# Performance work log

Measured on AMD Instinct MI355X. Metric: run time of the kernel, lower is better.

## Reference

```python
import jax, jax.numpy as jnp
import numpy as np

B, N, C, HEADS = 4, 8192, 512, 8


def setup_inputs() -> dict:
    key = jax.random.key(0)
    k1, k2, k3, k4, k5 = jax.random.split(key, 5)
    s = 1.0 / np.sqrt(C)
    return {
        "x": jax.random.normal(k1, (B, N, C), dtype=jnp.float32),
        "w_qkv": jax.random.normal(k2, (3 * C, C), dtype=jnp.float32) * s,
        "b_qkv": jax.random.normal(k3, (3 * C,), dtype=jnp.float32) * 0.01,
        "w_fc": jax.random.normal(k4, (C, C), dtype=jnp.float32) * s,
        "b_fc": jax.random.normal(k5, (C,), dtype=jnp.float32) * 0.01,
        "heads": HEADS,
    }


def reference(x, w_qkv, b_qkv, w_fc, b_fc, heads):
    b, n, c = x.shape
    d = c // heads
    scale = d ** (-0.5)
    # torch Linear: y = x @ W.T + b
    qkv = (x @ w_qkv.T + b_qkv).reshape(b, n, 3, heads, d)
    q, k, v = qkv[:, :, 0], qkv[:, :, 1], qkv[:, :, 2]  # [b,n,h,d]
    # NOTE: source does NOT move heads to dim 1, so attention is over the
    # heads axis: dots is [b, n, h, h].
    dots = jnp.einsum("bnhd,bngd->bnhg", q, k) * scale
    dots = jnp.clip(dots, -50.0, 50.0)
    attn = jax.nn.softmax(dots, axis=-1)
    out = jnp.einsum("bnhg,bngd->bnhd", attn, v)  # [b,n,h,d]
    # transpose(1,2).reshape(B,N,C) exactly as in torch (scrambles n/h)
    out = out.transpose(0, 2, 1, 3).reshape(b, n, c)
    return out @ w_fc.T + b_fc
```

## Files before the change

### kernel.cpp

```cpp
#include <hip/hip_runtime.h>
#include <hip/hip_bf16.h>
#include <stdint.h>


typedef __bf16 bf16x8 __attribute__((ext_vector_type(8)));
typedef float f32x4 __attribute__((ext_vector_type(4)));

__device__ __forceinline__ unsigned short f2bf(float f) {
  unsigned u = __float_as_uint(f);
  u += 0x7fffu + ((u >> 16) & 1u);
  return (unsigned short)(u >> 16);
}
__device__ __forceinline__ unsigned pk2(float a, float b) {
  return (unsigned)f2bf(a) | ((unsigned)f2bf(b) << 16);
}
__device__ __forceinline__ void unpk2(unsigned u, float& a, float& b) {
  a = __uint_as_float(u << 16);
  b = __uint_as_float(u & 0xffff0000u);
}

__device__ __forceinline__ void gload_lds16(const void* g, void* l) {
  __builtin_amdgcn_global_load_lds((const __attribute__((address_space(1))) void*)g,
                                   (__attribute__((address_space(3))) void*)l,
                                   16, 0, 0);
}

__global__ __launch_bounds__(256) void cvt_f32_to_bf16(const float* __restrict__ in,
                                                       __hip_bfloat16* __restrict__ out,
                                                       int n8) {
  int i = blockIdx.x * 256 + threadIdx.x;
  if (i >= n8) return;
  const float4* p = (const float4*)in;
  float4 a = p[i * 2];
  float4 b = p[i * 2 + 1];
  uint4 o;
  o.x = pk2(a.x, a.y);
  o.y = pk2(a.z, a.w);
  o.z = pk2(b.x, b.y);
  o.w = pk2(b.z, b.w);
  ((uint4*)out)[i] = o;
}

template <bool OUT_BF16>
__global__ __launch_bounds__(256) void gemm_bt(const __hip_bfloat16* __restrict__ A,
                                               const __hip_bfloat16* __restrict__ Bm,
                                               const float* __restrict__ bias,
                                               void* __restrict__ C,
                                               int M, int N, int K, int NT) {
  __shared__ __hip_bfloat16 sA[128 * 64];
  __shared__ __hip_bfloat16 sB[128 * 64];

  const int tid = threadIdx.x;
  const int wv = tid >> 6;
  const int ln = tid & 63;
  const int bid = blockIdx.x;
  const int mt = bid / NT, nt = bid % NT;
  const int bm0 = mt * 128, bn0 = nt * 128;
  const int lrow = ln & 15;
  const int kg = ln >> 4;
  const int wm = wv >> 1, wn = wv & 1;

  f32x4 acc[4][4] = {};

  int srow[4], scol[4], sbase[4];
  for (int i = 0; i < 4; ++i) {
    int ofs = (i * 4 + wv) * 1024 + ln * 16;
    srow[i] = ofs >> 7;
    scol[i] = (ofs & 127) >> 1;
    sbase[i] = (i * 4 + wv) * 512;
  }

  for (int k0 = 0; k0 < K; k0 += 64) {
    for (int i = 0; i < 4; ++i) {
      gload_lds16(A + (size_t)(bm0 + srow[i]) * K + k0 + scol[i], sA + sbase[i]);
      gload_lds16(Bm + (size_t)(bn0 + srow[i]) * K + k0 + scol[i], sB + sbase[i]);
    }
    __syncthreads();
#pragma unroll
    for (int ks = 0; ks < 2; ++ks) {
      bf16x8 af[4], bfr[4];
#pragma unroll
      for (int i = 0; i < 4; ++i) {
        af[i] = *(const bf16x8*)(sA + (wm * 64 + i * 16 + lrow) * 64 + ks * 32 + kg * 8);
        bfr[i] = *(const bf16x8*)(sB + (wn * 64 + i * 16 + lrow) * 64 + ks * 32 + kg * 8);
      }
#pragma unroll
      for (int i = 0; i < 4; ++i)
#pragma unroll
        for (int j = 0; j < 4; ++j)
          acc[i][j] = __builtin_amdgcn_mfma_f32_16x16x32_bf16(af[i], bfr[j], acc[i][j], 0, 0, 0);
    }
    __syncthreads();
  }

#pragma unroll
  for (int j = 0; j < 4; ++j) {
    int col = bn0 + wn * 64 + j * 16 + lrow;
    float bv = bias[col];
#pragma unroll
    for (int i = 0; i < 4; ++i) {
      int row0 = bm0 + wm * 64 + i * 16 + kg * 4;
#pragma unroll
      for (int r = 0; r < 4; ++r) {
        float v = acc[i][j][r] + bv;
        size_t idx = (size_t)(row0 + r) * N + col;
        if (OUT_BF16) {
          unsigned short us = f2bf(v);
          ((unsigned short*)C)[idx] = us;
        } else {
          ((float*)C)[idx] = v;
        }
      }
    }
  }
}

__global__ __launch_bounds__(256) void attn_tok(const __hip_bfloat16* __restrict__ qkv,
                                                __hip_bfloat16* __restrict__ outp,
                                                int ntok, int npb) {
  const int wv = threadIdx.x >> 6;
  const int ln = threadIdx.x & 63;
  const int t = blockIdx.x * 4 + wv;
  if (t >= ntok) return;
  const int m = ln & 7;

  const __hip_bfloat16* row = qkv + (size_t)t * 1536;
  uint4 qr = *(const uint4*)(row + ln * 8);
  uint4 kr = *(const uint4*)(row + 512 + ln * 8);
  uint4 vr = *(const uint4*)(row + 1024 + ln * 8);

  float qf[8];
  unpk2(qr.x, qf[0], qf[1]);
  unpk2(qr.y, qf[2], qf[3]);
  unpk2(qr.z, qf[4], qf[5]);
  unpk2(qr.w, qf[6], qf[7]);
  unsigned kw[4] = {kr.x, kr.y, kr.z, kr.w};
  unsigned vw[4] = {vr.x, vr.y, vr.z, vr.w};

  float dt[8];
#pragma unroll
  for (int g = 0; g < 8; ++g) {
    int src = g * 8 + m;
    float s = 0.f;
#pragma unroll
    for (int j4 = 0; j4 < 4; ++j4) {
      unsigned kk = __shfl(kw[j4], src, 64);
      float a, b;
      unpk2(kk, a, b);
      s += qf[j4 * 2] * a + qf[j4 * 2 + 1] * b;
    }
    s += __shfl_xor(s, 1, 64);
    s += __shfl_xor(s, 2, 64);
    s += __shfl_xor(s, 4, 64);
    dt[g] = s;
  }

  float mx = -1e30f;
#pragma unroll
  for (int g = 0; g < 8; ++g) {
    dt[g] = fminf(fmaxf(dt[g] * 0.125f, -50.f), 50.f);
    mx = fmaxf(mx, dt[g]);
  }
  float p[8], ssum = 0.f;
#pragma unroll
  for (int g = 0; g < 8; ++g) {
    p[g] = __expf(dt[g] - mx);
    ssum += p[g];
  }
  float inv = 1.f / ssum;

  float o[8] = {0, 0, 0, 0, 0, 0, 0, 0};
#pragma unroll
  for (int g = 0; g < 8; ++g) {
    int src = g * 8 + m;
    float ag = p[g] * inv;
#pragma unroll
    for (int j4 = 0; j4 < 4; ++j4) {
      unsigned vv = __shfl(vw[j4], src, 64);
      float a, b;
      unpk2(vv, a, b);
      o[j4 * 2] += ag * a;
      o[j4 * 2 + 1] += ag * b;
    }
  }

  const int h = ln >> 3;
  const int b = t / npb, n = t % npb;
  size_t dst = (size_t)b * npb * 512 + (size_t)(h * (npb >> 3) + (n >> 3)) * 512 +
               (size_t)((n & 7) * 64 + m * 8);
  uint4 ov;
  ov.x = pk2(o[0], o[1]);
  ov.y = pk2(o[2], o[3]);
  ov.z = pk2(o[4], o[5]);
  ov.w = pk2(o[6], o[7]);
  *(uint4*)(outp + dst) = ov;
}

extern "C" void kernel_launch(void* const* d_in, const int* in_sizes, int n_in,
                              void* d_out, int out_size, void* d_ws, size_t ws_size,
                              hipStream_t stream) {
  const float* x = (const float*)d_in[0];
  const float* w_qkv = (const float*)d_in[1];
  const float* b_qkv = (const float*)d_in[2];
  const float* w_fc = (const float*)d_in[3];
  const float* b_fc = (const float*)d_in[4];
  float* out = (float*)d_out;

  const int M = 32768;
  const int Cc = 512, N3 = 1536;

  __hip_bfloat16* xb = (__hip_bfloat16*)d_ws;
  __hip_bfloat16* wqkvb = xb + (size_t)M * Cc;
  __hip_bfloat16* wfcb = wqkvb + (size_t)N3 * Cc;
  __hip_bfloat16* qkvb = wfcb + (size_t)Cc * Cc;
  __hip_bfloat16* attb = qkvb + (size_t)M * N3;

  cvt_f32_to_bf16<<<(M * Cc / 8) / 256, 256, 0, stream>>>(x, xb, M * Cc / 8);
  cvt_f32_to_bf16<<<(N3 * Cc / 8) / 256, 256, 0, stream>>>(w_qkv, wqkvb, N3 * Cc / 8);
  cvt_f32_to_bf16<<<(Cc * Cc / 8) / 256, 256, 0, stream>>>(w_fc, wfcb, Cc * Cc / 8);

  gemm_bt<true><<<(M / 128) * (N3 / 128), 256, 0, stream>>>(xb, wqkvb, b_qkv, qkvb, M, N3, Cc,
                                                            N3 / 128);
  attn_tok<<<M / 4, 256, 0, stream>>>(qkvb, attb, M, 8192);
  gemm_bt<false><<<(M / 128) * (Cc / 128), 256, 0, stream>>>(attb, wfcb, b_fc, out, M, Cc, Cc,
                                                             Cc / 128);
}
```

Baseline: 181.9 us.

## Replace GEMM with 256x256 eight-wave double-buffered pipelined MFMA kernel

Both GEMMs now use a new kernel with 256x256 tiles, 512 threads (8 waves) and 128 KB of LDS holding two stages. Global-to-LDS loads for later k-tiles are interleaved with MFMA phases, using explicit barriers, waitcnts and priority hints. It also adds an XOR-swizzled LDS layout to avoid bank conflicts and a workgroup remap across XCDs. The aim is to hide memory latency and raise MFMA utilisation, at the cost of fewer workgroups: the fc GEMM launches only 256 blocks, and the large LDS footprint limits occupancy.

```diff
diff --git a/kernel.cpp b/kernel.cpp
--- a/kernel.cpp
+++ b/kernel.cpp
@@ -18,7 +18,6 @@
   a = __uint_as_float(u << 16);
   b = __uint_as_float(u & 0xffff0000u);
 }
-
 __device__ __forceinline__ void gload_lds16(const void* g, void* l) {
   __builtin_amdgcn_global_load_lds((const __attribute__((address_space(1))) void*)g,
                                    (__attribute__((address_space(3))) void*)l,
@@ -41,72 +40,134 @@
   ((uint4*)out)[i] = o;
 }
 
+
+#define STAGEH(SBUF, ISA, SKH, KT)                                                        \
+  do {                                                                                    \
+    const __hip_bfloat16* _sp = (ISA) ? Ag : Bg;                                          \
+    int _r0 = (ISA) ? bm0 : bn0;                                                          \
+    _Pragma("unroll") for (int _j = 0; _j < 2; ++_j) {                                    \
+      gload_lds16(_sp + (size_t)(_r0 + srow[_j]) * K + (KT) * 64 + (SKH) * 32 + skoff[_j],\
+                  lds + (SBUF) * 65536 + ((ISA) ? 0 : 32768) + (SKH) * 16384 +            \
+                      destoff[_j]);                                                       \
+    }                                                                                     \
+  } while (0)
+
+#define PHASE(BUF, KS, FH, SBUF, SISA, SKH, KT, DOW)                                      \
+  do {                                                                                    \
+    const char* _ab = lds + (BUF) * 65536 + (KS) * 16384 + wm * 8192 + (FH) * 4096 + pbase;\
+    bf16x8 _af0 = *(const bf16x8*)(_ab);                                                  \
+    bf16x8 _af1 = *(const bf16x8*)(_ab + 1024);                                           \
+    bf16x8 _af2 = *(const bf16x8*)(_ab + 2048);                                           \
+    bf16x8 _af3 = *(const bf16x8*)(_ab + 3072);                                           \
+    if (FH == 0) {                                                                        \
+      const char* _bb = lds + (BUF) * 65536 + 32768 + (KS) * 16384 + wn * 4096 + pbase;   \
+      bfr[0] = *(const bf16x8*)(_bb);                                                     \
+      bfr[1] = *(const bf16x8*)(_bb + 1024);                                              \
+      bfr[2] = *(const bf16x8*)(_bb + 2048);                                              \
+      bfr[3] = *(const bf16x8*)(_bb + 3072);                                              \
+    }                                                                                     \
+    STAGEH(SBUF, SISA, SKH, KT);                                                          \
+    __builtin_amdgcn_s_barrier();                                                         \
+    asm volatile("s_waitcnt lgkmcnt(0)" ::: "memory");                                    \
+    __builtin_amdgcn_sched_barrier(0);                                                    \
+    __builtin_amdgcn_s_setprio(1);                                                        \
+    _Pragma("unroll") for (int _c = 0; _c < 4; ++_c) {                                    \
+      acc[(FH) * 4 + 0][_c] =                                                             \
+          __builtin_amdgcn_mfma_f32_16x16x32_bf16(_af0, bfr[_c], acc[(FH) * 4 + 0][_c], 0, 0, 0); \
+      acc[(FH) * 4 + 1][_c] =                                                             \
+          __builtin_amdgcn_mfma_f32_16x16x32_bf16(_af1, bfr[_c], acc[(FH) * 4 + 1][_c], 0, 0, 0); \
+      acc[(FH) * 4 + 2][_c] =                                                             \
+          __builtin_amdgcn_mfma_f32_16x16x32_bf16(_af2, bfr[_c], acc[(FH) * 4 + 2][_c], 0, 0, 0); \
+      acc[(FH) * 4 + 3][_c] =                                                             \
+          __builtin_amdgcn_mfma_f32_16x16x32_bf16(_af3, bfr[_c], acc[(FH) * 4 + 3][_c], 0, 0, 0); \
+    }                                                                                     \
+    __builtin_amdgcn_s_setprio(0);                                                        \
+    if (DOW) {                                                                            \
+      asm volatile("s_waitcnt vmcnt(4)" ::: "memory");                                    \
+    }                                                                                     \
+    __builtin_amdgcn_s_barrier();                                                         \
+    __builtin_amdgcn_sched_barrier(0);                                                    \
+  } while (0)
+
 template <bool OUT_BF16>
-__global__ __launch_bounds__(256) void gemm_bt(const __hip_bfloat16* __restrict__ A,
-                                               const __hip_bfloat16* __restrict__ Bm,
-                                               const float* __restrict__ bias,
-                                               void* __restrict__ C,
-                                               int M, int N, int K, int NT) {
-  __shared__ __hip_bfloat16 sA[128 * 64];
-  __shared__ __hip_bfloat16 sB[128 * 64];
+__global__ __launch_bounds__(512, 2) void gemm8(const __hip_bfloat16* __restrict__ Ag,
+                                                const __hip_bfloat16* __restrict__ Bg,
+                                                const float* __restrict__ bias,
+                                                void* __restrict__ C,
+                                                int M, int N, int K, int NT) {
+  __shared__ char lds[131072];
 
   const int tid = threadIdx.x;
   const int wv = tid >> 6;
   const int ln = tid & 63;
-  const int bid = blockIdx.x;
-  const int mt = bid / NT, nt = bid % NT;
-  const int bm0 = mt * 128, bn0 = nt * 128;
   const int lrow = ln & 15;
   const int kg = ln >> 4;
-  const int wm = wv >> 1, wn = wv & 1;
-
-  f32x4 acc[4][4] = {};
-
-  int srow[4], scol[4], sbase[4];
-  for (int i = 0; i < 4; ++i) {
-    int ofs = (i * 4 + wv) * 1024 + ln * 16;
-    srow[i] = ofs >> 7;
-    scol[i] = (ofs & 127) >> 1;
-    sbase[i] = (i * 4 + wv) * 512;
-  }
-
-  for (int k0 = 0; k0 < K; k0 += 64) {
-    for (int i = 0; i < 4; ++i) {
-      gload_lds16(A + (size_t)(bm0 + srow[i]) * K + k0 + scol[i], sA + sbase[i]);
-      gload_lds16(Bm + (size_t)(bn0 + srow[i]) * K + k0 + scol[i], sB + sbase[i]);
-    }
-    __syncthreads();
-#pragma unroll
-    for (int ks = 0; ks < 2; ++ks) {
-      bf16x8 af[4], bfr[4];
-#pragma unroll
-      for (int i = 0; i < 4; ++i) {
-        af[i] = *(const bf16x8*)(sA + (wm * 64 + i * 16 + lrow) * 64 + ks * 32 + kg * 8);
-        bfr[i] = *(const bf16x8*)(sB + (wn * 64 + i * 16 + lrow) * 64 + ks * 32 + kg * 8);
-      }
-#pragma unroll
-      for (int i = 0; i < 4; ++i)
-#pragma unroll
-        for (int j = 0; j < 4; ++j)
-          acc[i][j] = __builtin_amdgcn_mfma_f32_16x16x32_bf16(af[i], bfr[j], acc[i][j], 0, 0, 0);
-    }
-    __syncthreads();
-  }
-
-#pragma unroll
-  for (int j = 0; j < 4; ++j) {
-    int col = bn0 + wn * 64 + j * 16 + lrow;
+  const int wm = wv >> 2;
+  const int wn = wv & 3;
+
+  int nwg = gridDim.x;
+  int cpx = nwg >> 3;
+  int bs = (blockIdx.x & 7) * cpx + (blockIdx.x >> 3);
+  const int bm0 = (bs / NT) * 256;
+  const int bn0 = (bs % NT) * 256;
+
+  const int pbase = (lrow >> 1) * 128 + ((((lrow & 1) << 2) | kg) ^ ((lrow >> 1) & 7)) * 16;
+
+  int srow[2], skoff[2], destoff[2];
+#pragma unroll
+  for (int j = 0; j < 2; ++j) {
+    int L = j * 8192 + wv * 1024 + ln * 16;
+    int rp = L >> 7;
+    int T = ((L >> 4) & 7) ^ (rp & 7);
+    srow[j] = rp * 2 + (T >> 2);
+    skoff[j] = (T & 3) * 8;
+    destoff[j] = j * 8192 + wv * 1024;
+  }
+
+  f32x4 acc[8][4] = {};
+  bf16x8 bfr[4];
+
+  const int NKT = K >> 6;
+  const int NI = NKT >> 1;
+
+  STAGEH(0, 1, 0, 0);
+  STAGEH(0, 0, 0, 0);
+  STAGEH(0, 1, 1, 0);
+  STAGEH(0, 0, 1, 0);
+  STAGEH(1, 1, 0, 1);
+  STAGEH(1, 0, 0, 1);
+  asm volatile("s_waitcnt vmcnt(4)" ::: "memory");
+  __builtin_amdgcn_s_barrier();
+  __builtin_amdgcn_sched_barrier(0);
+
+  for (int i = 0; i < NI; ++i) {
+    int kt1 = 2 * i + 1;
+    int kt2 = 2 * i + 2 < NKT ? 2 * i + 2 : NKT - 1;
+    int kt3 = 2 * i + 3 < NKT ? 2 * i + 3 : NKT - 1;
+    PHASE(0, 0, 0,  1, 1, 1, kt1, 0);
+    PHASE(0, 0, 1,  1, 0, 1, kt1, 0);
+    PHASE(0, 1, 0,  0, 1, 0, kt2, 0);
+    PHASE(0, 1, 1,  0, 0, 0, kt2, 1);
+    PHASE(1, 0, 0,  0, 1, 1, kt2, 0);
+    PHASE(1, 0, 1,  0, 0, 1, kt2, 0);
+    PHASE(1, 1, 0,  1, 1, 0, kt3, 0);
+    PHASE(1, 1, 1,  1, 0, 0, kt3, 1);
+  }
+  asm volatile("s_waitcnt vmcnt(0)" ::: "memory");
+
+#pragma unroll
+  for (int cj = 0; cj < 4; ++cj) {
+    int col = bn0 + wn * 64 + cj * 16 + lrow;
     float bv = bias[col];
 #pragma unroll
-    for (int i = 0; i < 4; ++i) {
-      int row0 = bm0 + wm * 64 + i * 16 + kg * 4;
+    for (int fi = 0; fi < 8; ++fi) {
+      int row0 = bm0 + wm * 128 + fi * 16 + kg * 4;
 #pragma unroll
       for (int r = 0; r < 4; ++r) {
-        float v = acc[i][j][r] + bv;
+        float v = acc[fi][cj][r] + bv;
         size_t idx = (size_t)(row0 + r) * N + col;
         if (OUT_BF16) {
-          unsigned short us = f2bf(v);
-          ((unsigned short*)C)[idx] = us;
+          ((unsigned short*)C)[idx] = f2bf(v);
         } else {
           ((float*)C)[idx] = v;
         }
@@ -219,9 +280,9 @@
   cvt_f32_to_bf16<<<(N3 * Cc / 8) / 256, 256, 0, stream>>>(w_qkv, wqkvb, N3 * Cc / 8);
   cvt_f32_to_bf16<<<(Cc * Cc / 8) / 256, 256, 0, stream>>>(w_fc, wfcb, Cc * Cc / 8);
 
-  gemm_bt<true><<<(M / 128) * (N3 / 128), 256, 0, stream>>>(xb, wqkvb, b_qkv, qkvb, M, N3, Cc,
-                                                            N3 / 128);
+  gemm8<true><<<(M / 256) * (N3 / 256), 512, 0, stream>>>(xb, wqkvb, b_qkv, qkvb, M, N3, Cc,
+                                                          N3 / 256);
   attn_tok<<<M / 4, 256, 0, stream>>>(qkvb, attb, M, 8192);
-  gemm_bt<false><<<(M / 128) * (Cc / 128), 256, 0, stream>>>(attb, wfcb, b_fc, out, M, Cc, Cc,
-                                                             Cc / 128);
-}
+  gemm8<false><<<(M / 256) * (Cc / 256), 512, 0, stream>>>(attb, wfcb, b_fc, out, M, Cc, Cc,
+                                                           Cc / 256);
+}
```

Result: faster. 168.0 us (-7.6%).

## Rewrite GEMMs with double-buffered swizzled LDS, larger tiles, and coalesced epilogue

Applied to the files above, without the earlier changes.

Replaces the single-buffered 128x128 GEMM with a 512-thread, 256x128-tile kernel. It prefetches the next 32-wide K slice into a second LDS buffer while the current one feeds MFMAs, and uses an XOR-swizzled LDS layout to avoid bank conflicts. Block IDs are remapped across 8 groups, probably for XCD-aware locality. Results are staged through LDS for vectorized, coalesced stores. This adds more LDS use and synchronization and uses a narrower K step per iteration.

```diff
diff --git a/kernel.cpp b/kernel.cpp
--- a/kernel.cpp
+++ b/kernel.cpp
@@ -18,7 +18,6 @@
   a = __uint_as_float(u << 16);
   b = __uint_as_float(u & 0xffff0000u);
 }
-
 __device__ __forceinline__ void gload_lds16(const void* g, void* l) {
   __builtin_amdgcn_global_load_lds((const __attribute__((address_space(1))) void*)g,
                                    (__attribute__((address_space(3))) void*)l,
@@ -41,76 +40,163 @@
   ((uint4*)out)[i] = o;
 }
 
+
+#define STG(S, BUF)                                                                       \
+  do {                                                                                    \
+    int _k0 = (S) * 32;                                                                   \
+    gload_lds16(Ag + (size_t)(bm0 + srowA0) * K + _k0 + skofA0,                           \
+                lds + (BUF) * 24576 + dstA0);                                             \
+    gload_lds16(Ag + (size_t)(bm0 + srowA1) * K + _k0 + skofA1,                           \
+                lds + (BUF) * 24576 + dstA1);                                             \
+    gload_lds16(Bg + (size_t)(bn0 + srowB) * K + _k0 + skofB,                             \
+                lds + (BUF) * 24576 + 16384 + dstB);                                      \
+  } while (0)
+
 template <bool OUT_BF16>
-__global__ __launch_bounds__(256) void gemm_bt(const __hip_bfloat16* __restrict__ A,
-                                               const __hip_bfloat16* __restrict__ Bm,
-                                               const float* __restrict__ bias,
-                                               void* __restrict__ C,
-                                               int M, int N, int K, int NT) {
-  __shared__ __hip_bfloat16 sA[128 * 64];
-  __shared__ __hip_bfloat16 sB[128 * 64];
+__global__ __launch_bounds__(512, 4) void gemm2p(const __hip_bfloat16* __restrict__ Ag,
+                                                 const __hip_bfloat16* __restrict__ Bg,
+                                                 const float* __restrict__ bias,
+                                                 void* __restrict__ C,
+                                                 int M, int N, int K, int NT) {
+  __shared__ __align__(16) char lds[65536];
 
   const int tid = threadIdx.x;
   const int wv = tid >> 6;
   const int ln = tid & 63;
-  const int bid = blockIdx.x;
-  const int mt = bid / NT, nt = bid % NT;
-  const int bm0 = mt * 128, bn0 = nt * 128;
   const int lrow = ln & 15;
   const int kg = ln >> 4;
-  const int wm = wv >> 1, wn = wv & 1;
+  const int wm = wv >> 1;
+  const int wn = wv & 1;
+
+  int nwg = gridDim.x;
+  int cpx = nwg >> 3;
+  int bs = (blockIdx.x & 7) * cpx + (blockIdx.x >> 3);
+  const int bm0 = (bs / NT) * 256;
+  const int bn0 = (bs % NT) * 128;
+
+  const int pbase = (lrow >> 1) * 128 + ((((lrow & 1) << 2) | kg) ^ ((lrow >> 1) & 7)) * 16;
+
+  int srowA0, skofA0, dstA0, srowA1, skofA1, dstA1, srowB, skofB, dstB;
+  {
+    int L0 = wv * 1024 + ln * 16;
+    int rp0 = L0 >> 7, T0 = ((L0 >> 4) & 7) ^ (rp0 & 7);
+    srowA0 = rp0 * 2 + (T0 >> 2);
+    skofA0 = (T0 & 3) * 8;
+    dstA0 = wv * 1024;
+    int L1 = 8192 + L0;
+    int rp1 = L1 >> 7, T1 = ((L1 >> 4) & 7) ^ (rp1 & 7);
+    srowA1 = rp1 * 2 + (T1 >> 2);
+    skofA1 = (T1 & 3) * 8;
+    dstA1 = 8192 + wv * 1024;
+    srowB = srowA0;
+    skofB = skofA0;
+    dstB = wv * 1024;
+  }
 
   f32x4 acc[4][4] = {};
 
-  int srow[4], scol[4], sbase[4];
-  for (int i = 0; i < 4; ++i) {
-    int ofs = (i * 4 + wv) * 1024 + ln * 16;
-    srow[i] = ofs >> 7;
-    scol[i] = (ofs & 127) >> 1;
-    sbase[i] = (i * 4 + wv) * 512;
-  }
-
-  for (int k0 = 0; k0 < K; k0 += 64) {
-    for (int i = 0; i < 4; ++i) {
-      gload_lds16(A + (size_t)(bm0 + srow[i]) * K + k0 + scol[i], sA + sbase[i]);
-      gload_lds16(Bm + (size_t)(bn0 + srow[i]) * K + k0 + scol[i], sB + sbase[i]);
-    }
-    __syncthreads();
-#pragma unroll
-    for (int ks = 0; ks < 2; ++ks) {
-      bf16x8 af[4], bfr[4];
-#pragma unroll
-      for (int i = 0; i < 4; ++i) {
-        af[i] = *(const bf16x8*)(sA + (wm * 64 + i * 16 + lrow) * 64 + ks * 32 + kg * 8);
-        bfr[i] = *(const bf16x8*)(sB + (wn * 64 + i * 16 + lrow) * 64 + ks * 32 + kg * 8);
-      }
-#pragma unroll
-      for (int i = 0; i < 4; ++i)
-#pragma unroll
-        for (int j = 0; j < 4; ++j)
-          acc[i][j] = __builtin_amdgcn_mfma_f32_16x16x32_bf16(af[i], bfr[j], acc[i][j], 0, 0, 0);
-    }
-    __syncthreads();
-  }
-
-#pragma unroll
-  for (int j = 0; j < 4; ++j) {
-    int col = bn0 + wn * 64 + j * 16 + lrow;
-    float bv = bias[col];
-#pragma unroll
-    for (int i = 0; i < 4; ++i) {
-      int row0 = bm0 + wm * 64 + i * 16 + kg * 4;
-#pragma unroll
-      for (int r = 0; r < 4; ++r) {
-        float v = acc[i][j][r] + bv;
-        size_t idx = (size_t)(row0 + r) * N + col;
-        if (OUT_BF16) {
-          unsigned short us = f2bf(v);
-          ((unsigned short*)C)[idx] = us;
-        } else {
-          ((float*)C)[idx] = v;
+  const int NKT = K >> 5;
+
+  STG(0, 0);
+  asm volatile("s_waitcnt vmcnt(0)" ::: "memory");
+  __builtin_amdgcn_s_barrier();
+  __builtin_amdgcn_sched_barrier(0);
+
+  for (int s = 0; s < NKT; ++s) {
+    int b = s & 1;
+    if (s + 1 < NKT) STG(s + 1, b ^ 1);
+    {
+      const char* _ab = lds + b * 24576 + wm * 4096 + pbase;
+      const char* _bb = lds + b * 24576 + 16384 + wn * 4096 + pbase;
+      bf16x8 a0 = *(const bf16x8*)(_ab);
+      bf16x8 a1 = *(const bf16x8*)(_ab + 1024);
+      bf16x8 a2 = *(const bf16x8*)(_ab + 2048);
+      bf16x8 a3 = *(const bf16x8*)(_ab + 3072);
+      bf16x8 b0 = *(const bf16x8*)(_bb);
+      bf16x8 b1 = *(const bf16x8*)(_bb + 1024);
+      bf16x8 b2 = *(const bf16x8*)(_bb + 2048);
+      bf16x8 b3 = *(const bf16x8*)(_bb + 3072);
+      asm volatile("s_waitcnt lgkmcnt(0)" ::: "memory");
+      __builtin_amdgcn_sched_barrier(0);
+      __builtin_amdgcn_s_setprio(1);
+      acc[0][0] = __builtin_amdgcn_mfma_f32_16x16x32_bf16(a0, b0, acc[0][0], 0, 0, 0);
+      acc[0][1] = __builtin_amdgcn_mfma_f32_16x16x32_bf16(a0, b1, acc[0][1], 0, 0, 0);
+      acc[0][2] = __builtin_amdgcn_mfma_f32_16x16x32_bf16(a0, b2, acc[0][2], 0, 0, 0);
+      acc[0][3] = __builtin_amdgcn_mfma_f32_16x16x32_bf16(a0, b3, acc[0][3], 0, 0, 0);
+      acc[1][0] = __builtin_amdgcn_mfma_f32_16x16x32_bf16(a1, b0, acc[1][0], 0, 0, 0);
+      acc[1][1] = __builtin_amdgcn_mfma_f32_16x16x32_bf16(a1, b1, acc[1][1], 0, 0, 0);
+      acc[1][2] = __builtin_amdgcn_mfma_f32_16x16x32_bf16(a1, b2, acc[1][2], 0, 0, 0);
+      acc[1][3] = __builtin_amdgcn_mfma_f32_16x16x32_bf16(a1, b3, acc[1][3], 0, 0, 0);
+      acc[2][0] = __builtin_amdgcn_mfma_f32_16x16x32_bf16(a2, b0, acc[2][0], 0, 0, 0);
+      acc[2][1] = __builtin_amdgcn_mfma_f32_16x16x32_bf16(a2, b1, acc[2][1], 0, 0, 0);
+      acc[2][2] = __builtin_amdgcn_mfma_f32_16x16x32_bf16(a2, b2, acc[2][2], 0, 0, 0);
+      acc[2][3] = __builtin_amdgcn_mfma_f32_16x16x32_bf16(a2, b3, acc[2][3], 0, 0, 0);
+      acc[3][0] = __builtin_amdgcn_mfma_f32_16x16x32_bf16(a3, b0, acc[3][0], 0, 0, 0);
+      acc[3][1] = __builtin_amdgcn_mfma_f32_16x16x32_bf16(a3, b1, acc[3][1], 0, 0, 0);
+      acc[3][2] = __builtin_amdgcn_mfma_f32_16x16x32_bf16(a3, b2, acc[3][2], 0, 0, 0);
+      acc[3][3] = __builtin_amdgcn_mfma_f32_16x16x32_bf16(a3, b3, acc[3][3], 0, 0, 0);
+      __builtin_amdgcn_s_setprio(0);
+    }
+    asm volatile("s_waitcnt vmcnt(0)" ::: "memory");
+    __builtin_amdgcn_s_barrier();
+    __builtin_amdgcn_sched_barrier(0);
+  }
+
+  if (OUT_BF16) {
+    unsigned short* tile = (unsigned short*)lds;
+#pragma unroll
+    for (int fi = 0; fi < 4; ++fi) {
+#pragma unroll
+      for (int cj = 0; cj < 4; ++cj) {
+        int col = wn * 64 + cj * 16 + lrow;
+        float bv = bias[bn0 + col];
+#pragma unroll
+        for (int r = 0; r < 4; ++r) {
+          int row = wm * 64 + fi * 16 + kg * 4 + r;
+          int sc = (((col >> 3) ^ (row & 7)) << 3) | (col & 7);
+          tile[row * 128 + sc] = f2bf(acc[fi][cj][r] + bv);
         }
       }
+    }
+    __syncthreads();
+#pragma unroll
+    for (int it = 0; it < 8; ++it) {
+      int id = it * 512 + tid;
+      int row = id >> 4;
+      int c = id & 15;
+      uint4 v = *(const uint4*)(lds + row * 256 + ((c ^ (row & 7)) << 4));
+      *(uint4*)((unsigned short*)C + (size_t)(bm0 + row) * N + bn0 + c * 8) = v;
+    }
+  } else {
+    float* tilef = (float*)lds;
+#pragma unroll
+    for (int pass = 0; pass < 2; ++pass) {
+      if ((wm >> 1) == pass) {
+#pragma unroll
+        for (int fi = 0; fi < 4; ++fi) {
+#pragma unroll
+          for (int cj = 0; cj < 4; ++cj) {
+            int col = wn * 64 + cj * 16 + lrow;
+            float bv = bias[bn0 + col];
+#pragma unroll
+            for (int r = 0; r < 4; ++r) {
+              int row = (wm & 1) * 64 + fi * 16 + kg * 4 + r;
+              int sc = (((col >> 2) ^ (row & 7)) << 2) | (col & 3);
+              tilef[row * 128 + sc] = acc[fi][cj][r] + bv;
+            }
+          }
+        }
+      }
+      __syncthreads();
+#pragma unroll
+      for (int it = 0; it < 8; ++it) {
+        int id = it * 512 + tid;
+        int row = id >> 5;
+        int c = id & 31;
+        uint4 v = *(const uint4*)(lds + row * 512 + ((c ^ (row & 7)) << 4));
+        *(uint4*)((float*)C + (size_t)(bm0 + pass * 128 + row) * N + bn0 + c * 4) = v;
+      }
+      __syncthreads();
     }
   }
 }
@@ -219,9 +305,9 @@
   cvt_f32_to_bf16<<<(N3 * Cc / 8) / 256, 256, 0, stream>>>(w_qkv, wqkvb, N3 * Cc / 8);
   cvt_f32_to_bf16<<<(Cc * Cc / 8) / 256, 256, 0, stream>>>(w_fc, wfcb, Cc * Cc / 8);
 
-  gemm_bt<true><<<(M / 128) * (N3 / 128), 256, 0, stream>>>(xb, wqkvb, b_qkv, qkvb, M, N3, Cc,
-                                                            N3 / 128);
+  gemm2p<true><<<(M / 256) * (N3 / 128), 512, 0, stream>>>(xb, wqkvb, b_qkv, qkvb, M, N3, Cc,
+                                                           N3 / 128);
   attn_tok<<<M / 4, 256, 0, stream>>>(qkvb, attb, M, 8192);
-  gemm_bt<false><<<(M / 128) * (Cc / 128), 256, 0, stream>>>(attb, wfcb, b_fc, out, M, Cc, Cc,
-                                                             Cc / 128);
-}
+  gemm2p<false><<<(M / 256) * (Cc / 128), 512, 0, stream>>>(attb, wfcb, b_fc, out, M, Cc, Cc,
+                                                            Cc / 128);
+}
```

Measured after the change: 152.4 us. -16.2%, faster.
